# Optimization experiments

Hardware: AMD Instinct MI355X
Metric: run time of the kernel (lower is better)

The kernel has to match this reference:

```python
import jax, jax.numpy as jnp
import numpy as np
import math

B, N, E, D = 4, 8192, 1024, 64

def setup_inputs() -> dict:
    key = jax.random.key(0)
    kx, kq, kk, kv, ko = jax.random.split(key, 5)
    x = jax.random.normal(kx, (B, N, E), dtype=jnp.float32)
    # ImplicitLinear weights: hash-generated Rademacher-like values scaled by 1/sqrt(in_features).
    # We stand in with sign(normal) * scale, matching the statistics of v_mask_generative * scale.
    wq = jnp.sign(jax.random.normal(kq, (D, E), dtype=jnp.float32)) / math.sqrt(E)
    wk = jnp.sign(jax.random.normal(kk, (D, E), dtype=jnp.float32)) / math.sqrt(E)
    wv = jnp.sign(jax.random.normal(kv, (D, E), dtype=jnp.float32)) / math.sqrt(E)
    wo = jnp.sign(jax.random.normal(ko, (E, D), dtype=jnp.float32)) / math.sqrt(D)
    return {"x": x, "wq": wq, "wk": wk, "wv": wv, "wo": wo}

def reference(x, wq, wk, wv, wo):
    # Projections: ImplicitLinear computes x @ W.T with W shaped [out, in]
    Q = jnp.einsum('bne,de->bnd', x, wq)   # [B,N,D]
    K = jnp.einsum('bne,de->bnd', x, wk)   # [B,N,D]
    V = jnp.einsum('bne,de->bnd', x, wv)   # [B,N,D]
    # ground mode: linear attention, energy = K^T @ V  -> [B,D,D]
    energy = jnp.einsum('bnd,bne->bde', K, V)
    context = jnp.einsum('bnd,bde->bne', Q, energy)  # [B,N,D]
    context = context * jnp.asarray(math.sqrt(3.0 / D), dtype=context.dtype)
    out = jnp.einsum('bnd,ed->bne', context, wo)  # [B,N,E]
    return out
```

## Files before the change

### kernel.cpp

```cpp
#include <hip/hip_runtime.h>
#include <hip/hip_bf16.h>
#include <stdint.h>


typedef __bf16 bf16x8 __attribute__((ext_vector_type(8)));
typedef float  f32x4  __attribute__((ext_vector_type(4)));

#define MFMA_BF16(A, Bb, C) __builtin_amdgcn_mfma_f32_16x16x32_bf16(A, Bb, C, 0, 0, 0)

__device__ __forceinline__ int swz8(int row, int slot) { return (slot ^ (row & 7)) << 3; }

__device__ __forceinline__ void gload_lds16(const void* g, void* l) {
    __builtin_amdgcn_global_load_lds(
        (const __attribute__((address_space(1))) unsigned int*)g,
        (__attribute__((address_space(3))) unsigned int*)l, 16, 0, 0);
}

__global__ __launch_bounds__(128) void prep_kernel(
    const float* __restrict__ wq, const float* __restrict__ wk,
    const float* __restrict__ wv, const float* __restrict__ wo,
    __bf16* __restrict__ Wb)
{
    const int gid = blockIdx.x * 128 + threadIdx.x;
    const int e0  = gid * 8;
    const float* src = (e0 < 65536)  ? wq + e0
                     : (e0 < 131072) ? wk + (e0 - 65536)
                     : (e0 < 196608) ? wv + (e0 - 131072)
                                     : wo + (e0 - 196608);
    float w[8];
    *(float4*)&w[0] = *(const float4*)(src);
    *(float4*)&w[4] = *(const float4*)(src + 4);
    bf16x8 wb;
#pragma unroll
    for (int j = 0; j < 8; ++j) wb[j] = (__bf16)w[j];
    *(bf16x8*)&Wb[e0] = wb;
}

__global__ __launch_bounds__(256) void qkv_kernel(
    const float* __restrict__ x, const __bf16* __restrict__ Wb,
    float* __restrict__ Qf, float* __restrict__ Kf, float* __restrict__ Vf)
{
    __shared__ __bf16 xh[2][32 * 64];
    __shared__ __bf16 xl[2][32 * 64];

    const int tid  = threadIdx.x;
    const int lane = tid & 63;
    const int wid  = tid >> 6;
    const int lr   = lane & 15;
    const int kg   = lane >> 4;
    const int row0 = blockIdx.x * 32;

    const int sr = tid >> 3;
    const int f8 = tid & 7;

    f32x4 acc[2][3];
#pragma unroll
    for (int i = 0; i < 2; ++i)
#pragma unroll
        for (int j = 0; j < 3; ++j) acc[i][j] = (f32x4){0.f, 0.f, 0.f, 0.f};

    float xv[8], xn[8];

#define LOAD_X(dst, stp)                                                        \
    {                                                                           \
        const float* src_ = &x[(size_t)(row0 + sr) * 1024 + (stp) * 64 + f8 * 8]; \
        *(float4*)&dst[0] = *(const float4*)(src_);                             \
        *(float4*)&dst[4] = *(const float4*)(src_ + 4);                         \
    }

    LOAD_X(xv, 0);

#pragma unroll 2
    for (int step = 0; step < 16; ++step) {
        const int cur = step & 1;
        {
            bf16x8 h, l;
#pragma unroll
            for (int j = 0; j < 8; ++j) {
                const float v = xv[j];
                const unsigned int bb = __float_as_uint(v);
                h[j] = __builtin_bit_cast(__bf16, (unsigned short)(bb >> 16));
                l[j] = (__bf16)(v - __uint_as_float(bb & 0xffff0000u));
            }
            const int off = sr * 64 + swz8(sr, f8);
            *(bf16x8*)&xh[cur][off] = h;
            *(bf16x8*)&xl[cur][off] = l;
        }
        __syncthreads();
        if (step < 15) LOAD_X(xn, step + 1);

#pragma unroll
        for (int ks = 0; ks < 2; ++ks) {
            const int slot = ks * 4 + kg;
            bf16x8 Ah[2], Al[2], Bw[3];
#pragma unroll
            for (int am = 0; am < 2; ++am) {
                const int row = am * 16 + lr;
                Ah[am] = *(const bf16x8*)&xh[cur][row * 64 + swz8(row, slot)];
                Al[am] = *(const bf16x8*)&xl[cur][row * 64 + swz8(row, slot)];
            }
#pragma unroll
            for (int bn = 0; bn < 3; ++bn) {
                const int col = wid * 48 + bn * 16 + lr;
                Bw[bn] = *(const bf16x8*)&Wb[(size_t)col * 1024 + step * 64 + slot * 8];
            }
#pragma unroll
            for (int am = 0; am < 2; ++am)
#pragma unroll
                for (int bn = 0; bn < 3; ++bn) {
                    acc[am][bn] = MFMA_BF16(Ah[am], Bw[bn], acc[am][bn]);
                    acc[am][bn] = MFMA_BF16(Al[am], Bw[bn], acc[am][bn]);
                }
        }
#pragma unroll
        for (int j = 0; j < 8; ++j) xv[j] = xn[j];
    }
#undef LOAD_X

#pragma unroll
    for (int am = 0; am < 2; ++am)
#pragma unroll
        for (int bn = 0; bn < 3; ++bn) {
            const int col  = wid * 48 + bn * 16 + lr;
            const int rowb = row0 + am * 16 + kg * 4;
            float* dst = (col < 64) ? Qf : (col < 128) ? Kf : Vf;
            const int cc = col & 63;
#pragma unroll
            for (int r = 0; r < 4; ++r)
                dst[(size_t)(rowb + r) * 64 + cc] = acc[am][bn][r];
        }
}

__global__ __launch_bounds__(512) void energy_partial_kernel(
    const float* __restrict__ Kf, const float* __restrict__ Vf,
    float* __restrict__ part)
{
    __shared__ float lK[32 * 64];
    __shared__ float lV[32 * 64];
    const int tid  = threadIdx.x;
    const int lane = tid & 63;
    const int wid  = tid >> 6;
    const int d    = tid >> 3;
    const int e0   = (tid & 7) * 8;
    const int row0 = blockIdx.x * 128;

    float acc[8] = {0.f, 0.f, 0.f, 0.f, 0.f, 0.f, 0.f, 0.f};

    for (int c = 0; c < 4; ++c) {
        const size_t boff = (size_t)(row0 + c * 32) * 256 + wid * 1024 + (lane << 4);
        gload_lds16((const char*)Kf + boff, (char*)lK + wid * 1024);
        gload_lds16((const char*)Vf + boff, (char*)lV + wid * 1024);
        __syncthreads();
        for (int n = 0; n < 32; ++n) {
            const float kv = lK[n * 64 + d];
            const float4 a = *(const float4*)&lV[n * 64 + e0];
            const float4 b = *(const float4*)&lV[n * 64 + e0 + 4];
            acc[0] += kv * a.x; acc[1] += kv * a.y; acc[2] += kv * a.z; acc[3] += kv * a.w;
            acc[4] += kv * b.x; acc[5] += kv * b.y; acc[6] += kv * b.z; acc[7] += kv * b.w;
        }
        __syncthreads();
    }
    float* p = part + (size_t)blockIdx.x * 4096 + d * 64 + e0;
    *(float4*)&p[0] = make_float4(acc[0], acc[1], acc[2], acc[3]);
    *(float4*)&p[4] = make_float4(acc[4], acc[5], acc[6], acc[7]);
}

__global__ __launch_bounds__(256) void energy_reduce_kernel(
    const float* __restrict__ part, __bf16* __restrict__ Eth, __bf16* __restrict__ Etl)
{
    const int b    = blockIdx.x >> 4;
    const int elem = ((blockIdx.x & 15) << 8) + threadIdx.x;
    float s = 0.f;
#pragma unroll 8
    for (int c = 0; c < 64; ++c)
        s += part[(size_t)(b * 64 + c) * 4096 + elem];
    s *= 0.2165063509461097f;
    const int d = elem >> 6, e = elem & 63;
    const __bf16 h = (__bf16)s;
    const __bf16 l = (__bf16)(s - (float)h);
    const size_t o = (size_t)b * 4096 + e * 64 + swz8(e, d >> 3) + (d & 7);
    Eth[o] = h; Etl[o] = l;
}

__global__ __launch_bounds__(512) void out_kernel(
    const float* __restrict__ Qf,
    const __bf16* __restrict__ Eth, const __bf16* __restrict__ Etl,
    const __bf16* __restrict__ Wob, float* __restrict__ out)
{
    __shared__ __bf16 qh[64 * 64];
    __shared__ __bf16 ql[64 * 64];
    __shared__ __bf16 ch[64 * 64];
    __shared__ __bf16 cl[64 * 64];

    const int tid  = threadIdx.x;
    const int lane = tid & 63;
    const int wid  = tid >> 6;
    const int lr   = lane & 15;
    const int kg   = lane >> 4;
    const int wm   = wid >> 2;
    const int wn   = wid & 3;
    const int row0 = blockIdx.x * 64;
    const int b    = blockIdx.x >> 7;

    {
        const int r  = tid >> 3;
        const int f8 = tid & 7;
        const float* src = &Qf[(size_t)(row0 + r) * 64 + f8 * 8];
        float v[8];
        *(float4*)&v[0] = *(const float4*)(src);
        *(float4*)&v[4] = *(const float4*)(src + 4);
        bf16x8 h, l;
#pragma unroll
        for (int j = 0; j < 8; ++j) {
            const unsigned int bb = __float_as_uint(v[j]);
            h[j] = __builtin_bit_cast(__bf16, (unsigned short)(bb >> 16));
            l[j] = (__bf16)(v[j] - __uint_as_float(bb & 0xffff0000u));
        }
        const int off = r * 64 + swz8(r, f8);
        *(bf16x8*)&qh[off] = h;
        *(bf16x8*)&ql[off] = l;
    }
    __syncthreads();

    f32x4 cacc[2];
    cacc[0] = (f32x4){0.f, 0.f, 0.f, 0.f};
    cacc[1] = (f32x4){0.f, 0.f, 0.f, 0.f};
#pragma unroll
    for (int ks = 0; ks < 2; ++ks) {
        const int slot = ks * 4 + kg;
        const int e    = wn * 16 + lr;
        const bf16x8 Bh = *(const bf16x8*)&Eth[(size_t)b * 4096 + e * 64 + swz8(e, slot)];
        const bf16x8 Bl = *(const bf16x8*)&Etl[(size_t)b * 4096 + e * 64 + swz8(e, slot)];
#pragma unroll
        for (int am = 0; am < 2; ++am) {
            const int row = wm * 32 + am * 16 + lr;
            const bf16x8 Ah = *(const bf16x8*)&qh[row * 64 + swz8(row, slot)];
            const bf16x8 Al = *(const bf16x8*)&ql[row * 64 + swz8(row, slot)];
            cacc[am] = MFMA_BF16(Ah, Bh, cacc[am]);
            cacc[am] = MFMA_BF16(Ah, Bl, cacc[am]);
            cacc[am] = MFMA_BF16(Al, Bh, cacc[am]);
        }
    }
#pragma unroll
    for (int am = 0; am < 2; ++am)
#pragma unroll
        for (int r = 0; r < 4; ++r) {
            const int n  = wm * 32 + am * 16 + kg * 4 + r;
            const int dd = wn * 16 + lr;
            const float v  = cacc[am][r];
            const __bf16 h = (__bf16)v;
            const __bf16 l = (__bf16)(v - (float)h);
            const int off = n * 64 + swz8(n, dd >> 3) + (dd & 7);
            ch[off] = h; cl[off] = l;
        }
    __syncthreads();

    bf16x8 Ah[2][2], Al[2][2];
#pragma unroll
    for (int am = 0; am < 2; ++am)
#pragma unroll
        for (int ks = 0; ks < 2; ++ks) {
            const int row  = wm * 32 + am * 16 + lr;
            const int slot = ks * 4 + kg;
            Ah[am][ks] = *(const bf16x8*)&ch[row * 64 + swz8(row, slot)];
            Al[am][ks] = *(const bf16x8*)&cl[row * 64 + swz8(row, slot)];
        }
#pragma unroll
    for (int g = 0; g < 4; ++g) {
        f32x4 oacc[2][4];
#pragma unroll
        for (int i = 0; i < 2; ++i)
#pragma unroll
            for (int j = 0; j < 4; ++j) oacc[i][j] = (f32x4){0.f, 0.f, 0.f, 0.f};
#pragma unroll
        for (int ks = 0; ks < 2; ++ks) {
            bf16x8 Bw[4];
#pragma unroll
            for (int bn = 0; bn < 4; ++bn) {
                const int col = wn * 256 + g * 64 + bn * 16 + lr;
                Bw[bn] = *(const bf16x8*)&Wob[(size_t)col * 64 + ks * 32 + kg * 8];
            }
#pragma unroll
            for (int am = 0; am < 2; ++am)
#pragma unroll
                for (int bn = 0; bn < 4; ++bn) {
                    oacc[am][bn] = MFMA_BF16(Ah[am][ks], Bw[bn], oacc[am][bn]);
                    oacc[am][bn] = MFMA_BF16(Al[am][ks], Bw[bn], oacc[am][bn]);
                }
        }
#pragma unroll
        for (int am = 0; am < 2; ++am)
#pragma unroll
            for (int bn = 0; bn < 4; ++bn) {
                const int gcol = wn * 256 + g * 64 + bn * 16 + lr;
                const int grow = row0 + wm * 32 + am * 16 + kg * 4;
#pragma unroll
                for (int r = 0; r < 4; ++r)
                    __builtin_nontemporal_store(oacc[am][bn][r],
                        &out[(size_t)(grow + r) * 1024 + gcol]);
            }
    }
}

extern "C" void kernel_launch(void* const* d_in, const int* in_sizes, int n_in,
                              void* d_out, int out_size, void* d_ws, size_t ws_size,
                              hipStream_t stream)
{
    const float* x  = (const float*)d_in[0];
    const float* wq = (const float*)d_in[1];
    const float* wk = (const float*)d_in[2];
    const float* wv = (const float*)d_in[3];
    const float* wo = (const float*)d_in[4];
    float* out = (float*)d_out;

    char* ws = (char*)d_ws;
    float*  Qf   = (float*)(ws);
    float*  Kf   = (float*)(ws + 8388608);
    float*  Vf   = (float*)(ws + 16777216);
    float*  part = (float*)(ws + 25165824);
    __bf16* Wb   = (__bf16*)(ws + 29360128);
    __bf16* Wob  = (__bf16*)(ws + 29753344);
    __bf16* Eth  = (__bf16*)(ws + 30408704);
    __bf16* Etl  = (__bf16*)(ws + 30441472);

    prep_kernel<<<256, 128, 0, stream>>>(wq, wk, wv, wo, Wb);
    qkv_kernel<<<1024, 256, 0, stream>>>(x, Wb, Qf, Kf, Vf);
    energy_partial_kernel<<<256, 512, 0, stream>>>(Kf, Vf, part);
    energy_reduce_kernel<<<64, 256, 0, stream>>>(part, Eth, Etl);
    out_kernel<<<512, 512, 0, stream>>>(Qf, Eth, Etl, Wob, out);
}
```

Before: 309.0 us.

## Split context and output projection into separate kernels and deepen x prefetch

The fused output kernel becomes two kernels. A ctx kernel computes Q·energy and writes the context to global memory as split bf16 hi/lo halves. A separate out kernel, launched over 4096 smaller blocks, does the Wo projection to spread the output GEMM more widely. The qkv kernel now prefetches x two steps ahead, issues weight loads earlier and uses a waitcnt-plus-barrier instead of __syncthreads. Energy partials use 64-row blocks with 16 accumulators per thread and plain loads into shared memory. The split adds a global round trip for the context and an extra launch.

Measured after the change: 338.1 us. 9.4% more time.

```diff
diff --git a/kernel.cpp b/kernel.cpp
--- a/kernel.cpp
+++ b/kernel.cpp
@@ -10,10 +10,9 @@
 
 __device__ __forceinline__ int swz8(int row, int slot) { return (slot ^ (row & 7)) << 3; }
 
-__device__ __forceinline__ void gload_lds16(const void* g, void* l) {
-    __builtin_amdgcn_global_load_lds(
-        (const __attribute__((address_space(1))) unsigned int*)g,
-        (__attribute__((address_space(3))) unsigned int*)l, 16, 0, 0);
+__device__ __forceinline__ void lds_barrier() {
+    asm volatile("s_waitcnt lgkmcnt(0)" ::: "memory");
+    __builtin_amdgcn_s_barrier();
 }
 
 __global__ __launch_bounds__(128) void prep_kernel(
@@ -49,9 +48,8 @@
     const int lr   = lane & 15;
     const int kg   = lane >> 4;
     const int row0 = blockIdx.x * 32;
-
-    const int sr = tid >> 3;
-    const int f8 = tid & 7;
+    const int sr   = tid >> 3;
+    const int f8   = tid & 7;
 
     f32x4 acc[2][3];
 #pragma unroll
@@ -59,18 +57,20 @@
 #pragma unroll
         for (int j = 0; j < 3; ++j) acc[i][j] = (f32x4){0.f, 0.f, 0.f, 0.f};
 
-    float xv[8], xn[8];
-
-#define LOAD_X(dst, stp)                                                        \
-    {                                                                           \
-        const float* src_ = &x[(size_t)(row0 + sr) * 1024 + (stp) * 64 + f8 * 8]; \
-        *(float4*)&dst[0] = *(const float4*)(src_);                             \
-        *(float4*)&dst[4] = *(const float4*)(src_ + 4);                         \
+    const float* xbase = &x[(size_t)(row0 + sr) * 1024 + f8 * 8];
+    float xv[8], xn[8], xm[8];
+#pragma unroll
+    for (int j = 0; j < 8; ++j) xm[j] = 0.f;
+
+#define LOAD_X(dst, stp)                                                       \
+    {                                                                          \
+        *(float4*)&dst[0] = *(const float4*)(xbase + (stp) * 64);              \
+        *(float4*)&dst[4] = *(const float4*)(xbase + (stp) * 64 + 4);          \
     }
 
     LOAD_X(xv, 0);
-
-#pragma unroll 2
+    LOAD_X(xn, 1);
+
     for (int step = 0; step < 16; ++step) {
         const int cur = step & 1;
         {
@@ -86,13 +86,18 @@
             *(bf16x8*)&xh[cur][off] = h;
             *(bf16x8*)&xl[cur][off] = l;
         }
-        __syncthreads();
-        if (step < 15) LOAD_X(xn, step + 1);
+        lds_barrier();
+        if (step < 14) LOAD_X(xm, step + 2);
 
 #pragma unroll
         for (int ks = 0; ks < 2; ++ks) {
             const int slot = ks * 4 + kg;
             bf16x8 Ah[2], Al[2], Bw[3];
+#pragma unroll
+            for (int bn = 0; bn < 3; ++bn) {
+                const int col = wid * 48 + bn * 16 + lr;
+                Bw[bn] = *(const bf16x8*)&Wb[(size_t)col * 1024 + step * 64 + slot * 8];
+            }
 #pragma unroll
             for (int am = 0; am < 2; ++am) {
                 const int row = am * 16 + lr;
@@ -100,11 +105,6 @@
                 Al[am] = *(const bf16x8*)&xl[cur][row * 64 + swz8(row, slot)];
             }
 #pragma unroll
-            for (int bn = 0; bn < 3; ++bn) {
-                const int col = wid * 48 + bn * 16 + lr;
-                Bw[bn] = *(const bf16x8*)&Wb[(size_t)col * 1024 + step * 64 + slot * 8];
-            }
-#pragma unroll
             for (int am = 0; am < 2; ++am)
 #pragma unroll
                 for (int bn = 0; bn < 3; ++bn) {
@@ -113,7 +113,7 @@
                 }
         }
 #pragma unroll
-        for (int j = 0; j < 8; ++j) xv[j] = xn[j];
+        for (int j = 0; j < 8; ++j) { xv[j] = xn[j]; xn[j] = xm[j]; }
     }
 #undef LOAD_X
 
@@ -131,38 +131,46 @@
         }
 }
 
-__global__ __launch_bounds__(512) void energy_partial_kernel(
+__global__ __launch_bounds__(256) void energy_partial_kernel(
     const float* __restrict__ Kf, const float* __restrict__ Vf,
     float* __restrict__ part)
 {
-    __shared__ float lK[32 * 64];
-    __shared__ float lV[32 * 64];
+    __shared__ float lK[64 * 64];
+    __shared__ float lV[64 * 64];
     const int tid  = threadIdx.x;
-    const int lane = tid & 63;
-    const int wid  = tid >> 6;
-    const int d    = tid >> 3;
-    const int e0   = (tid & 7) * 8;
-    const int row0 = blockIdx.x * 128;
-
-    float acc[8] = {0.f, 0.f, 0.f, 0.f, 0.f, 0.f, 0.f, 0.f};
-
-    for (int c = 0; c < 4; ++c) {
-        const size_t boff = (size_t)(row0 + c * 32) * 256 + wid * 1024 + (lane << 4);
-        gload_lds16((const char*)Kf + boff, (char*)lK + wid * 1024);
-        gload_lds16((const char*)Vf + boff, (char*)lV + wid * 1024);
-        __syncthreads();
-        for (int n = 0; n < 32; ++n) {
-            const float kv = lK[n * 64 + d];
-            const float4 a = *(const float4*)&lV[n * 64 + e0];
-            const float4 b = *(const float4*)&lV[n * 64 + e0 + 4];
-            acc[0] += kv * a.x; acc[1] += kv * a.y; acc[2] += kv * a.z; acc[3] += kv * a.w;
-            acc[4] += kv * b.x; acc[5] += kv * b.y; acc[6] += kv * b.z; acc[7] += kv * b.w;
-        }
-        __syncthreads();
-    }
-    float* p = part + (size_t)blockIdx.x * 4096 + d * 64 + e0;
-    *(float4*)&p[0] = make_float4(acc[0], acc[1], acc[2], acc[3]);
-    *(float4*)&p[4] = make_float4(acc[4], acc[5], acc[6], acc[7]);
+    const int row0 = blockIdx.x * 64;
+
+#pragma unroll
+    for (int i = 0; i < 4; ++i) {
+        const int idx = tid + i * 256;
+        const int r   = idx >> 4;
+        const int c4  = (idx & 15) << 2;
+        *(float4*)&lK[r * 64 + c4] = *(const float4*)&Kf[(size_t)(row0 + r) * 64 + c4];
+        *(float4*)&lV[r * 64 + c4] = *(const float4*)&Vf[(size_t)(row0 + r) * 64 + c4];
+    }
+    __syncthreads();
+
+    const int d  = tid & 63;
+    const int eb = (tid >> 6) * 16;
+    float acc[16];
+#pragma unroll
+    for (int j = 0; j < 16; ++j) acc[j] = 0.f;
+
+    for (int n = 0; n < 64; ++n) {
+        const float kd = lK[n * 64 + d];
+        const float4 v0 = *(const float4*)&lV[n * 64 + eb];
+        const float4 v1 = *(const float4*)&lV[n * 64 + eb + 4];
+        const float4 v2 = *(const float4*)&lV[n * 64 + eb + 8];
+        const float4 v3 = *(const float4*)&lV[n * 64 + eb + 12];
+        acc[0]  += kd * v0.x; acc[1]  += kd * v0.y; acc[2]  += kd * v0.z; acc[3]  += kd * v0.w;
+        acc[4]  += kd * v1.x; acc[5]  += kd * v1.y; acc[6]  += kd * v1.z; acc[7]  += kd * v1.w;
+        acc[8]  += kd * v2.x; acc[9]  += kd * v2.y; acc[10] += kd * v2.z; acc[11] += kd * v2.w;
+        acc[12] += kd * v3.x; acc[13] += kd * v3.y; acc[14] += kd * v3.z; acc[15] += kd * v3.w;
+    }
+    float* p = part + (size_t)blockIdx.x * 4096 + d * 64 + eb;
+#pragma unroll
+    for (int i = 0; i < 4; ++i)
+        *(float4*)&p[i * 4] = make_float4(acc[i*4], acc[i*4+1], acc[i*4+2], acc[i*4+3]);
 }
 
 __global__ __launch_bounds__(256) void energy_reduce_kernel(
@@ -172,134 +180,136 @@
     const int elem = ((blockIdx.x & 15) << 8) + threadIdx.x;
     float s = 0.f;
 #pragma unroll 8
-    for (int c = 0; c < 64; ++c)
-        s += part[(size_t)(b * 64 + c) * 4096 + elem];
+    for (int c = 0; c < 128; ++c)
+        s += part[(size_t)(b * 128 + c) * 4096 + elem];
     s *= 0.2165063509461097f;
     const int d = elem >> 6, e = elem & 63;
     const __bf16 h = (__bf16)s;
     const __bf16 l = (__bf16)(s - (float)h);
-    const size_t o = (size_t)b * 4096 + e * 64 + swz8(e, d >> 3) + (d & 7);
+    const size_t o = (size_t)b * 4096 + e * 64 + d;
     Eth[o] = h; Etl[o] = l;
 }
 
-__global__ __launch_bounds__(512) void out_kernel(
+__global__ __launch_bounds__(256) void ctx_kernel(
     const float* __restrict__ Qf,
     const __bf16* __restrict__ Eth, const __bf16* __restrict__ Etl,
-    const __bf16* __restrict__ Wob, float* __restrict__ out)
-{
-    __shared__ __bf16 qh[64 * 64];
-    __shared__ __bf16 ql[64 * 64];
-    __shared__ __bf16 ch[64 * 64];
-    __shared__ __bf16 cl[64 * 64];
+    __bf16* __restrict__ Ch, __bf16* __restrict__ Cl)
+{
+    __shared__ float ct[4][16 * 68];
 
     const int tid  = threadIdx.x;
     const int lane = tid & 63;
     const int wid  = tid >> 6;
     const int lr   = lane & 15;
     const int kg   = lane >> 4;
-    const int wm   = wid >> 2;
-    const int wn   = wid & 3;
-    const int row0 = blockIdx.x * 64;
+    const int row0 = blockIdx.x * 64 + wid * 16;
     const int b    = blockIdx.x >> 7;
 
-    {
-        const int r  = tid >> 3;
-        const int f8 = tid & 7;
-        const float* src = &Qf[(size_t)(row0 + r) * 64 + f8 * 8];
-        float v[8];
-        *(float4*)&v[0] = *(const float4*)(src);
-        *(float4*)&v[4] = *(const float4*)(src + 4);
-        bf16x8 h, l;
+    bf16x8 Qh[2], Ql[2];
+#pragma unroll
+    for (int ks = 0; ks < 2; ++ks) {
+        float qv[8];
+        const float* src = &Qf[(size_t)(row0 + lr) * 64 + (ks * 4 + kg) * 8];
+        *(float4*)&qv[0] = *(const float4*)(src);
+        *(float4*)&qv[4] = *(const float4*)(src + 4);
 #pragma unroll
         for (int j = 0; j < 8; ++j) {
-            const unsigned int bb = __float_as_uint(v[j]);
-            h[j] = __builtin_bit_cast(__bf16, (unsigned short)(bb >> 16));
-            l[j] = (__bf16)(v[j] - __uint_as_float(bb & 0xffff0000u));
-        }
-        const int off = r * 64 + swz8(r, f8);
-        *(bf16x8*)&qh[off] = h;
-        *(bf16x8*)&ql[off] = l;
-    }
-    __syncthreads();
-
-    f32x4 cacc[2];
-    cacc[0] = (f32x4){0.f, 0.f, 0.f, 0.f};
-    cacc[1] = (f32x4){0.f, 0.f, 0.f, 0.f};
+            const unsigned int bb = __float_as_uint(qv[j]);
+            Qh[ks][j] = __builtin_bit_cast(__bf16, (unsigned short)(bb >> 16));
+            Ql[ks][j] = (__bf16)(qv[j] - __uint_as_float(bb & 0xffff0000u));
+        }
+    }
+
+    f32x4 cacc[4];
+#pragma unroll
+    for (int i = 0; i < 4; ++i) cacc[i] = (f32x4){0.f, 0.f, 0.f, 0.f};
+
 #pragma unroll
     for (int ks = 0; ks < 2; ++ks) {
         const int slot = ks * 4 + kg;
-        const int e    = wn * 16 + lr;
-        const bf16x8 Bh = *(const bf16x8*)&Eth[(size_t)b * 4096 + e * 64 + swz8(e, slot)];
-        const bf16x8 Bl = *(const bf16x8*)&Etl[(size_t)b * 4096 + e * 64 + swz8(e, slot)];
-#pragma unroll
-        for (int am = 0; am < 2; ++am) {
-            const int row = wm * 32 + am * 16 + lr;
-            const bf16x8 Ah = *(const bf16x8*)&qh[row * 64 + swz8(row, slot)];
-            const bf16x8 Al = *(const bf16x8*)&ql[row * 64 + swz8(row, slot)];
-            cacc[am] = MFMA_BF16(Ah, Bh, cacc[am]);
-            cacc[am] = MFMA_BF16(Ah, Bl, cacc[am]);
-            cacc[am] = MFMA_BF16(Al, Bh, cacc[am]);
-        }
-    }
-#pragma unroll
-    for (int am = 0; am < 2; ++am)
-#pragma unroll
-        for (int r = 0; r < 4; ++r) {
-            const int n  = wm * 32 + am * 16 + kg * 4 + r;
-            const int dd = wn * 16 + lr;
-            const float v  = cacc[am][r];
-            const __bf16 h = (__bf16)v;
-            const __bf16 l = (__bf16)(v - (float)h);
-            const int off = n * 64 + swz8(n, dd >> 3) + (dd & 7);
-            ch[off] = h; cl[off] = l;
-        }
+#pragma unroll
+        for (int eb = 0; eb < 4; ++eb) {
+            const int e = eb * 16 + lr;
+            const bf16x8 Bh = *(const bf16x8*)&Eth[(size_t)b * 4096 + e * 64 + slot * 8];
+            const bf16x8 Bl = *(const bf16x8*)&Etl[(size_t)b * 4096 + e * 64 + slot * 8];
+            cacc[eb] = MFMA_BF16(Qh[ks], Bh, cacc[eb]);
+            cacc[eb] = MFMA_BF16(Qh[ks], Bl, cacc[eb]);
+            cacc[eb] = MFMA_BF16(Ql[ks], Bh, cacc[eb]);
+        }
+    }
+
+#pragma unroll
+    for (int eb = 0; eb < 4; ++eb)
+#pragma unroll
+        for (int r = 0; r < 4; ++r)
+            ct[wid][(kg * 4 + r) * 68 + eb * 16 + lr] = cacc[eb][r];
     __syncthreads();
 
-    bf16x8 Ah[2][2], Al[2][2];
-#pragma unroll
-    for (int am = 0; am < 2; ++am)
-#pragma unroll
-        for (int ks = 0; ks < 2; ++ks) {
-            const int row  = wm * 32 + am * 16 + lr;
-            const int slot = ks * 4 + kg;
-            Ah[am][ks] = *(const bf16x8*)&ch[row * 64 + swz8(row, slot)];
-            Al[am][ks] = *(const bf16x8*)&cl[row * 64 + swz8(row, slot)];
-        }
-#pragma unroll
-    for (int g = 0; g < 4; ++g) {
-        f32x4 oacc[2][4];
-#pragma unroll
-        for (int i = 0; i < 2; ++i)
-#pragma unroll
-            for (int j = 0; j < 4; ++j) oacc[i][j] = (f32x4){0.f, 0.f, 0.f, 0.f};
-#pragma unroll
-        for (int ks = 0; ks < 2; ++ks) {
-            bf16x8 Bw[4];
-#pragma unroll
-            for (int bn = 0; bn < 4; ++bn) {
-                const int col = wn * 256 + g * 64 + bn * 16 + lr;
-                Bw[bn] = *(const bf16x8*)&Wob[(size_t)col * 64 + ks * 32 + kg * 8];
-            }
-#pragma unroll
-            for (int am = 0; am < 2; ++am)
-#pragma unroll
-                for (int bn = 0; bn < 4; ++bn) {
-                    oacc[am][bn] = MFMA_BF16(Ah[am][ks], Bw[bn], oacc[am][bn]);
-                    oacc[am][bn] = MFMA_BF16(Al[am][ks], Bw[bn], oacc[am][bn]);
-                }
-        }
-#pragma unroll
-        for (int am = 0; am < 2; ++am)
-#pragma unroll
-            for (int bn = 0; bn < 4; ++bn) {
-                const int gcol = wn * 256 + g * 64 + bn * 16 + lr;
-                const int grow = row0 + wm * 32 + am * 16 + kg * 4;
-#pragma unroll
-                for (int r = 0; r < 4; ++r)
-                    __builtin_nontemporal_store(oacc[am][bn][r],
-                        &out[(size_t)(grow + r) * 1024 + gcol]);
-            }
-    }
+    const int r2 = lane >> 2;
+    const int c8 = (lane & 3) * 16;
+    float f[16];
+#pragma unroll
+    for (int i = 0; i < 4; ++i)
+        *(float4*)&f[i * 4] = *(const float4*)&ct[wid][r2 * 68 + c8 + i * 4];
+    bf16x8 h[2], l[2];
+#pragma unroll
+    for (int g = 0; g < 2; ++g)
+#pragma unroll
+        for (int j = 0; j < 8; ++j) {
+            const float v = f[g * 8 + j];
+            const unsigned int bb = __float_as_uint(v);
+            h[g][j] = __builtin_bit_cast(__bf16, (unsigned short)(bb >> 16));
+            l[g][j] = (__bf16)(v - __uint_as_float(bb & 0xffff0000u));
+        }
+    const size_t o = (size_t)(row0 + r2) * 64 + c8;
+    *(bf16x8*)&Ch[o]     = h[0];
+    *(bf16x8*)&Ch[o + 8] = h[1];
+    *(bf16x8*)&Cl[o]     = l[0];
+    *(bf16x8*)&Cl[o + 8] = l[1];
+}
+
+__global__ __launch_bounds__(256) void out_kernel(
+    const __bf16* __restrict__ Ch, const __bf16* __restrict__ Cl,
+    const __bf16* __restrict__ Wob, float* __restrict__ out)
+{
+    const int tid  = threadIdx.x;
+    const int lane = tid & 63;
+    const int wid  = tid >> 6;
+    const int lr   = lane & 15;
+    const int kg   = lane >> 4;
+    const int row0 = (blockIdx.x >> 1) * 16;
+    const int c0   = (blockIdx.x & 1) * 512 + wid * 128;
+
+    bf16x8 Ah[2], Al[2];
+#pragma unroll
+    for (int ks = 0; ks < 2; ++ks) {
+        const size_t o = (size_t)(row0 + lr) * 64 + (ks * 4 + kg) * 8;
+        Ah[ks] = *(const bf16x8*)&Ch[o];
+        Al[ks] = *(const bf16x8*)&Cl[o];
+    }
+
+    f32x4 oacc[8];
+#pragma unroll
+    for (int i = 0; i < 8; ++i) oacc[i] = (f32x4){0.f, 0.f, 0.f, 0.f};
+
+#pragma unroll
+    for (int ks = 0; ks < 2; ++ks) {
+        const int slot = ks * 4 + kg;
+#pragma unroll
+        for (int bn = 0; bn < 8; ++bn) {
+            const int col = c0 + bn * 16 + lr;
+            const bf16x8 Bw = *(const bf16x8*)&Wob[(size_t)col * 64 + slot * 8];
+            oacc[bn] = MFMA_BF16(Ah[ks], Bw, oacc[bn]);
+            oacc[bn] = MFMA_BF16(Al[ks], Bw, oacc[bn]);
+        }
+    }
+
+#pragma unroll
+    for (int bn = 0; bn < 8; ++bn)
+#pragma unroll
+        for (int r = 0; r < 4; ++r)
+            __builtin_nontemporal_store(oacc[bn][r],
+                &out[(size_t)(row0 + kg * 4 + r) * 1024 + c0 + bn * 16 + lr]);
 }
 
 extern "C" void kernel_launch(void* const* d_in, const int* in_sizes, int n_in,
@@ -318,14 +328,17 @@
     float*  Kf   = (float*)(ws + 8388608);
     float*  Vf   = (float*)(ws + 16777216);
     float*  part = (float*)(ws + 25165824);
-    __bf16* Wb   = (__bf16*)(ws + 29360128);
-    __bf16* Wob  = (__bf16*)(ws + 29753344);
-    __bf16* Eth  = (__bf16*)(ws + 30408704);
-    __bf16* Etl  = (__bf16*)(ws + 30441472);
+    __bf16* Wb   = (__bf16*)(ws + 33554432);
+    __bf16* Wob  = Wb + 196608;
+    __bf16* Eth  = (__bf16*)(ws + 34603008);
+    __bf16* Etl  = (__bf16*)(ws + 34635776);
+    __bf16* Ch   = (__bf16*)(ws + 34668544);
+    __bf16* Cl   = (__bf16*)(ws + 38862848);
 
     prep_kernel<<<256, 128, 0, stream>>>(wq, wk, wv, wo, Wb);
     qkv_kernel<<<1024, 256, 0, stream>>>(x, Wb, Qf, Kf, Vf);
-    energy_partial_kernel<<<256, 512, 0, stream>>>(Kf, Vf, part);
+    energy_partial_kernel<<<512, 256, 0, stream>>>(Kf, Vf, part);
     energy_reduce_kernel<<<64, 256, 0, stream>>>(part, Eth, Etl);
-    out_kernel<<<512, 512, 0, stream>>>(Qf, Eth, Etl, Wob, out);
-}
+    ctx_kernel<<<512, 256, 0, stream>>>(Qf, Eth, Etl, Ch, Cl);
+    out_kernel<<<4096, 256, 0, stream>>>(Ch, Cl, Wob, out);
+}
```
